# Kernel tuning notes

Measured on AMD Instinct MI355X. Metric: run time of the kernel, lower is better.

## Reference

```python
import jax, jax.numpy as jnp
import numpy as np
from jax.scipy.special import gammaln

N_L, N_Q, D_IN, D_CTX, H, MAX_AGENT = 256, 65536, 384, 192, 64, 6
STD2 = 0.1
VAR2 = STD2 * STD2
LOG_VAR2 = float(np.log(VAR2))
TEMP = 1.0


def _linear_init(k, out_dim, in_dim):
    k1, k2 = jax.random.split(k)
    s = 1.0 / np.sqrt(in_dim)
    w = jax.random.uniform(k1, (out_dim, in_dim), minval=-s, maxval=s, dtype=jnp.float32)
    b = jax.random.uniform(k2, (out_dim,), minval=-s, maxval=s, dtype=jnp.float32)
    return w, b


def setup_inputs() -> dict:
    key = jax.random.key(0)
    ks = jax.random.split(key, 12)
    fc1_w, fc1_b = _linear_init(ks[0], H, D_IN)
    fc21_w, fc21_b = _linear_init(ks[1], H, H)
    fc22_w, fc22_b = _linear_init(ks[2], H, H)
    fc3_w, fc3_b = _linear_init(ks[3], H, H)
    fc4_w, fc4_b = _linear_init(ks[4], D_IN, H)
    ctx_w, ctx_b = _linear_init(ks[5], H, D_CTX)
    llms = jax.random.normal(ks[6], (N_L, D_IN), dtype=jnp.float32)
    contexts = jax.random.normal(ks[7], (N_Q, D_CTX), dtype=jnp.float32)
    agent_num_int = jax.random.randint(ks[8], (N_Q, 1), 1, MAX_AGENT + 1, dtype=jnp.int32)
    agent_num_float = agent_num_int.astype(jnp.float32)
    noise_eps = jax.random.normal(ks[9], (N_L, H), dtype=jnp.float32)   # VAE reparameterize eps
    rand_u = jax.random.uniform(ks[10], (MAX_AGENT, N_Q, 1), dtype=jnp.float32)  # per-step uniforms
    return dict(llms=llms, contexts=contexts, agent_num_int=agent_num_int,
                agent_num_float=agent_num_float,
                fc1_w=fc1_w, fc1_b=fc1_b, fc21_w=fc21_w, fc21_b=fc21_b,
                fc22_w=fc22_w, fc22_b=fc22_b, fc3_w=fc3_w, fc3_b=fc3_b,
                fc4_w=fc4_w, fc4_b=fc4_b, ctx_w=ctx_w, ctx_b=ctx_b,
                noise_eps=noise_eps, rand_u=rand_u)


def _l2norm(x):
    n = jnp.sqrt(jnp.sum(x * x, axis=1, keepdims=True))
    return x / jnp.maximum(n, 1e-12)


def reference(llms, contexts, agent_num_int, agent_num_float,
              fc1_w, fc1_b, fc21_w, fc21_b, fc22_w, fc22_b,
              fc3_w, fc3_b, fc4_w, fc4_b, ctx_w, ctx_b, noise_eps, rand_u):
    # ---- VAE encode / reparameterize / decode ----
    h = jax.nn.relu(llms @ fc1_w.T + fc1_b)
    mu = h @ fc21_w.T + fc21_b
    log_var = h @ fc22_w.T + fc22_b
    std = jnp.exp(0.5 * log_var) * STD2
    z = mu + noise_eps * std
    h2 = jax.nn.relu(z @ fc3_w.T + fc3_b)
    x_hat = h2 @ fc4_w.T + fc4_b
    mse = jnp.mean((x_hat - llms) ** 2)
    kld = -0.5 * jnp.mean(1.0 - LOG_VAR2 + log_var - (mu ** 2 + jnp.exp(log_var)) / VAR2)
    vae_loss = mse + kld

    # ---- embeddings and routing scores ----
    llm_emb = _l2norm(z)                                   # [N_l, H]
    ctx_emb = _l2norm(contexts @ ctx_w.T + ctx_b)          # [N_q, H]
    scores = jax.nn.softmax((ctx_emb @ llm_emb.T) / TEMP, axis=1)  # [N_q, N_l]
    scores_cumsum = jnp.cumsum(scores, axis=1)

    # ---- vectorized max_agent-step categorical sampling ----
    # sel[i, q] = first llm where cumsum > u (inverse-CDF sampling), for step i
    sel = jnp.argmax(scores_cumsum[None, :, :] > rand_u, axis=2)          # [A, N_q]
    steps = jnp.arange(1, rand_u.shape[0] + 1, dtype=agent_num_int.dtype)
    mask = (agent_num_int[None, :, 0] >= steps[:, None]).astype(scores.dtype)  # [A, N_q]
    rows = jnp.broadcast_to(jnp.arange(scores.shape[0])[None, :], sel.shape)
    selected_llm = jnp.zeros_like(scores).at[rows, sel].add(mask)          # [N_q, N_l]

    log_probs = (gammaln(agent_num_float + 1.0)
                 - jnp.sum(gammaln(selected_llm + 1.0), axis=1, keepdims=True)
                 + jnp.sum(selected_llm * jnp.log(scores), axis=1, keepdims=True))
    return selected_llm, log_probs, vae_loss
```

## Files before the change

kernel.cpp:

```cpp
#include <hip/hip_runtime.h>

#define N_L 256
#define N_Q 65536
#define D_IN 384
#define D_CTX 192
#define HDIM 64
#define MAXA 6

typedef float v2f __attribute__((ext_vector_type(2)));

__device__ __forceinline__ v2f mk2(float a, float b) { v2f r; r.x = a; r.y = b; return r; }

__device__ __forceinline__ void fma4(float& acc, const float4& w, const float4& v) {
    acc = fmaf(w.x, v.x, acc);
    acc = fmaf(w.y, v.y, acc);
    acc = fmaf(w.z, v.z, acc);
    acc = fmaf(w.w, v.w, acc);
}

__device__ __forceinline__ float lgfact(int n) {
    return (n <= 1) ? 0.0f :
           (n == 2) ? 0.6931471805599453f :
           (n == 3) ? 1.7917594692280550f :
           (n == 4) ? 3.1780538303479458f :
           (n == 5) ? 4.7874917427820460f :
                      6.5792512120101010f;
}

template<int CTRL, int RM, bool BC>
__device__ __forceinline__ float dppz(float x) {
    return __int_as_float(__builtin_amdgcn_update_dpp(0, __float_as_int(x), CTRL, RM, 0xF, BC));
}
template<int CTRL, int RM>
__device__ __forceinline__ float dpps(float x) {
    int xi = __float_as_int(x);
    return __int_as_float(__builtin_amdgcn_update_dpp(xi, xi, CTRL, RM, 0xF, false));
}
__device__ __forceinline__ float wave_iscan(float t) {
    t += dppz<0x111, 0xF, true>(t);
    t += dppz<0x112, 0xF, true>(t);
    t += dppz<0x114, 0xF, true>(t);
    t += dppz<0x118, 0xF, true>(t);
    t += dppz<0x142, 0xA, false>(t);
    t += dppz<0x143, 0xC, false>(t);
    return t;
}
__device__ __forceinline__ float wave_max_l63(float m) {
    m = fmaxf(m, dpps<0x111, 0xF>(m));
    m = fmaxf(m, dpps<0x112, 0xF>(m));
    m = fmaxf(m, dpps<0x114, 0xF>(m));
    m = fmaxf(m, dpps<0x118, 0xF>(m));
    m = fmaxf(m, dpps<0x142, 0xA>(m));
    m = fmaxf(m, dpps<0x143, 0xC>(m));
    return m;
}
__device__ __forceinline__ float bc63(float x) {
    return __int_as_float(__builtin_amdgcn_readlane(__float_as_int(x), 63));
}

__device__ __forceinline__ void pk_fma_lo(v2f& d, v2f a, v2f b) {
    asm("v_pk_fma_f32 %0, %1, %2, %0 op_sel:[0,0,0] op_sel_hi:[1,0,1]"
        : "+v"(d) : "v"(a), "v"(b));
}
__device__ __forceinline__ void pk_fma_hi(v2f& d, v2f a, v2f b) {
    asm("v_pk_fma_f32 %0, %1, %2, %0 op_sel:[0,1,0] op_sel_hi:[1,1,1]"
        : "+v"(d) : "v"(a), "v"(b));
}

__global__ __launch_bounds__(64) void vae_kernel(
    const float* __restrict__ llms, const float* __restrict__ ctx_w,
    const float* __restrict__ fc1_w, const float* __restrict__ fc1_b,
    const float* __restrict__ fc21_w, const float* __restrict__ fc21_b,
    const float* __restrict__ fc22_w, const float* __restrict__ fc22_b,
    const float* __restrict__ fc3_w, const float* __restrict__ fc3_b,
    const float* __restrict__ fc4_w, const float* __restrict__ fc4_b,
    const float* __restrict__ eps,
    float* __restrict__ ctx_wP, float* __restrict__ embT,
    float* __restrict__ mse_row, float* __restrict__ kld_row)
{
    __shared__ __align__(16) float xs[D_IN];
    __shared__ __align__(16) float hs[HDIM];
    __shared__ __align__(16) float zs[HDIM];
    __shared__ __align__(16) float h2s[HDIM];
    const int r = blockIdx.x;
    const int j = threadIdx.x;

    {
        int f = r * 64 + j;
        if (f < D_CTX * HDIM) {
            int p = f >> 2, rr = f & 3;
            int jc = p & 63, k4 = p >> 6;
            ctx_wP[f] = ctx_w[jc * D_CTX + k4 * 4 + rr];
        }
    }

    for (int k = j; k < D_IN; k += 64) xs[k] = llms[r * D_IN + k];
    __syncthreads();

    float acc = fc1_b[j];
    {
        const float4* wr = (const float4*)(fc1_w + (size_t)j * D_IN);
        const float4* xr = (const float4*)xs;
        #pragma unroll 8
        for (int k4 = 0; k4 < D_IN / 4; ++k4) { fma4(acc, wr[k4], xr[k4]); }
    }
    float h = fmaxf(acc, 0.0f);
    hs[j] = h;
    __syncthreads();

    float mu = fc21_b[j], lv = fc22_b[j];
    {
        const float4* w1 = (const float4*)(fc21_w + (size_t)j * HDIM);
        const float4* w2 = (const float4*)(fc22_w + (size_t)j * HDIM);
        const float4* hr = (const float4*)hs;
        #pragma unroll
        for (int k4 = 0; k4 < HDIM / 4; ++k4) {
            float4 hh = hr[k4];
            fma4(mu, w1[k4], hh);
            fma4(lv, w2[k4], hh);
        }
    }
    float stdv = expf(0.5f * lv) * 0.1f;
    float z = fmaf(eps[r * HDIM + j], stdv, mu);

    float elv = expf(lv);
    float kt = (1.0f - (-4.60517018598809136f)) + lv - (mu * mu + elv) / 0.01f;
    float ks = kt;
    #pragma unroll
    for (int o = 32; o; o >>= 1) ks += __shfl_xor(ks, o);

    float zsq = z * z;
    #pragma unroll
    for (int o = 32; o; o >>= 1) zsq += __shfl_xor(zsq, o);
    float nrm = fmaxf(sqrtf(zsq), 1e-12f);
    embT[j * N_L + r] = z / nrm;
    zs[j] = z;
    __syncthreads();

    float a3 = fc3_b[j];
    {
        const float4* w3 = (const float4*)(fc3_w + (size_t)j * HDIM);
        const float4* zr = (const float4*)zs;
        #pragma unroll
        for (int k4 = 0; k4 < HDIM / 4; ++k4) { fma4(a3, w3[k4], zr[k4]); }
    }
    float h2 = fmaxf(a3, 0.0f);
    h2s[j] = h2;
    __syncthreads();

    float ms = 0.0f;
    const float4* h2r = (const float4*)h2s;
    #pragma unroll
    for (int m = 0; m < 6; ++m) {
        int o = j + 64 * m;
        float a4 = fc4_b[o];
        const float4* w4 = (const float4*)(fc4_w + (size_t)o * HDIM);
        #pragma unroll
        for (int k4 = 0; k4 < HDIM / 4; ++k4) { fma4(a4, w4[k4], h2r[k4]); }
        float d = a4 - xs[o];
        ms = fmaf(d, d, ms);
    }
    #pragma unroll
    for (int o = 32; o; o >>= 1) ms += __shfl_xor(ms, o);
    if (j == 0) { mse_row[r] = ms; kld_row[r] = ks; }
}

__global__ __launch_bounds__(256) void route_kernel(
    const float* __restrict__ contexts, const float* __restrict__ ctx_wP, const float* __restrict__ ctx_b,
    const float* __restrict__ embT, const int* __restrict__ agent_num, const float* __restrict__ rand_u,
    const float* __restrict__ mse_row, const float* __restrict__ kld_row,
    float* __restrict__ out_sel, float* __restrict__ out_lp, float* __restrict__ out_loss)
{
    __shared__ __align__(16) float lds[4][1536];

    const int tid = threadIdx.x;
    const int lane = tid & 63;
    const int widx = tid >> 6;
    const int l0 = lane << 2;

    const int g = blockIdx.x * 4 + widx;
    const int q0 = __builtin_amdgcn_readfirstlane(g << 3);
    float* myl = lds[widx];

    {
        float4* xls = (float4*)myl;
        const float4* cbase = (const float4*)contexts + (size_t)q0 * (D_CTX / 4);
        #pragma unroll
        for (int it = 0; it < 6; ++it) {
            int f = lane + it * 64;
            xls[f] = cbase[f];
        }
    }

    if (g == 0) {
        int rr = lane * 4;
        float ms = mse_row[rr] + mse_row[rr + 1] + mse_row[rr + 2] + mse_row[rr + 3];
        float ks = kld_row[rr] + kld_row[rr + 1] + kld_row[rr + 2] + kld_row[rr + 3];
        #pragma unroll
        for (int o = 32; o; o >>= 1) { ms += __shfl_xor(ms, o); ks += __shfl_xor(ks, o); }
        if (lane == 0) out_loss[0] = ms / 98304.0f - 0.5f * (ks / 16384.0f);
    }

    int Aq[8];
    #pragma unroll
    for (int q = 0; q < 8; ++q) Aq[q] = agent_num[q0 + q];

    const float bj = ctx_b[lane];
    v2f acc[8];
    #pragma unroll
    for (int q = 0; q < 8; ++q) acc[q] = mk2(bj, 0.0f);
    {
        const float4* wp = (const float4*)ctx_wP;
        const float4* xls = (const float4*)myl;
        #pragma unroll 2
        for (int k4 = 0; k4 < D_CTX / 4; ++k4) {
            float4 w = wp[k4 * HDIM + lane];
            v2f w01 = mk2(w.x, w.y), w23 = mk2(w.z, w.w);
            #pragma unroll
            for (int q = 0; q < 8; ++q) {
                float4 xv = xls[q * 48 + k4];
                acc[q] = __builtin_elementwise_fma(w01, mk2(xv.x, xv.y), acc[q]);
                acc[q] = __builtin_elementwise_fma(w23, mk2(xv.z, xv.w), acc[q]);
            }
        }
    }
    float e[8];
    #pragma unroll
    for (int q = 0; q < 8; ++q) e[q] = acc[q].x + acc[q].y;
    #pragma unroll
    for (int q = 0; q < 8; ++q) {
        float s = bc63(wave_iscan(e[q] * e[q]));
        e[q] *= 1.0f / fmaxf(sqrtf(s), 1e-12f);
        myl[q * HDIM + lane] = e[q];
    }

    v2f Pa[8], Pb[8];
    #pragma unroll
    for (int q = 0; q < 8; ++q) { Pa[q] = mk2(0.0f, 0.0f); Pb[q] = mk2(0.0f, 0.0f); }

    #pragma unroll 2
    for (int j4 = 0; j4 < HDIM / 4; ++j4) {
        float4 M0 = *(const float4*)(embT + (size_t)(j4 * 4 + 0) * N_L + l0);
        float4 M1 = *(const float4*)(embT + (size_t)(j4 * 4 + 1) * N_L + l0);
        float4 M2 = *(const float4*)(embT + (size_t)(j4 * 4 + 2) * N_L + l0);
        float4 M3 = *(const float4*)(embT + (size_t)(j4 * 4 + 3) * N_L + l0);
        v2f m0a = mk2(M0.x, M0.y), m0b = mk2(M0.z, M0.w);
        v2f m1a = mk2(M1.x, M1.y), m1b = mk2(M1.z, M1.w);
        v2f m2a = mk2(M2.x, M2.y), m2b = mk2(M2.z, M2.w);
        v2f m3a = mk2(M3.x, M3.y), m3b = mk2(M3.z, M3.w);
        #pragma unroll
        for (int q = 0; q < 8; ++q) {
            float4 ev = *(const float4*)(myl + q * HDIM + j4 * 4);
            v2f e01 = mk2(ev.x, ev.y), e23 = mk2(ev.z, ev.w);
            pk_fma_lo(Pa[q], m0a, e01);
            pk_fma_hi(Pa[q], m1a, e01);
            pk_fma_lo(Pa[q], m2a, e23);
            pk_fma_hi(Pa[q], m3a, e23);
            pk_fma_lo(Pb[q], m0b, e01);
            pk_fma_hi(Pb[q], m1b, e01);
            pk_fma_lo(Pb[q], m2b, e23);
            pk_fma_hi(Pb[q], m3b, e23);
        }
    }

    float4 P[8];
    #pragma unroll
    for (int k = 0; k < 8; ++k) P[k] = make_float4(Pa[k].x, Pa[k].y, Pb[k].x, Pb[k].y);

    #pragma unroll
    for (int k = 0; k < 8; ++k) {
        float m = fmaxf(fmaxf(P[k].x, P[k].y), fmaxf(P[k].z, P[k].w));
        m = bc63(wave_max_l63(m));
        P[k].x = expf(P[k].x - m); P[k].y = expf(P[k].y - m);
        P[k].z = expf(P[k].z - m); P[k].w = expf(P[k].w - m);
        float s = bc63(wave_iscan(P[k].x + P[k].y + P[k].z + P[k].w));
        float inv = 1.0f / s;
        P[k].x *= inv; P[k].y *= inv; P[k].z *= inv; P[k].w *= inv;
    }

    float c0[8], c1[8], c2[8], c3[8];
    #pragma unroll
    for (int k = 0; k < 8; ++k) {
        c0[k] = P[k].x; c1[k] = c0[k] + P[k].y; c2[k] = c1[k] + P[k].z;
        float p3 = c2[k] + P[k].w;
        float t = wave_iscan(p3);
        float base = t - p3;
        c0[k] += base; c1[k] += base; c2[k] += base; c3[k] = p3 + base;
    }

    unsigned nib[8] = {0, 0, 0, 0, 0, 0, 0, 0};
    #pragma unroll
    for (int i = 0; i < MAXA; ++i) {
        #pragma unroll
        for (int k = 0; k < 8; ++k) {
            if (i < Aq[k]) {
                float u = rand_u[(size_t)i * N_Q + q0 + k];
                unsigned long long b0 = __ballot(c0[k] <= u);
                unsigned long long b1 = __ballot(c1[k] <= u);
                unsigned long long b2 = __ballot(c2[k] <= u);
                unsigned long long b3 = __ballot(c3[k] <= u);
                int loc = __popcll(b0) + __popcll(b1) + __popcll(b2) + __popcll(b3);
                int sel = (loc >= N_L) ? 0 : loc;
                unsigned d = (unsigned)(sel - l0);
                if (d < 4u) nib[k] += 1u << (4 * d);
            }
        }
    }

    float term[8];
    #pragma unroll
    for (int k = 0; k < 8; ++k) {
        int n0 = nib[k] & 15, n1 = (nib[k] >> 4) & 15, n2 = (nib[k] >> 8) & 15, n3 = (nib[k] >> 12) & 15;
        float4 rowv = make_float4((float)n0, (float)n1, (float)n2, (float)n3);
        *(((float4*)(out_sel + (size_t)(q0 + k) * N_L)) + lane) = rowv;
        float tm = 0.0f;
        if (n0) tm += (float)n0 * logf(P[k].x) - lgfact(n0);
        if (n1) tm += (float)n1 * logf(P[k].y) - lgfact(n1);
        if (n2) tm += (float)n2 * logf(P[k].z) - lgfact(n2);
        if (n3) tm += (float)n3 * logf(P[k].w) - lgfact(n3);
        term[k] = tm;
    }
    float st[8];
    #pragma unroll
    for (int k = 0; k < 8; ++k) st[k] = bc63(wave_iscan(term[k]));

    if (lane < 8) {
        float rr = st[0];
        int Aa = Aq[0];
        #pragma unroll
        for (int k = 1; k < 8; ++k) {
            if (lane == k) { rr = st[k]; Aa = Aq[k]; }
        }
        out_lp[q0 + lane] = lgfact(Aa) + rr;
    }
}

extern "C" void kernel_launch(void* const* d_in, const int* in_sizes, int n_in,
                              void* d_out, int out_size, void* d_ws, size_t ws_size,
                              hipStream_t stream) {
    const float* llms      = (const float*)d_in[0];
    const float* contexts  = (const float*)d_in[1];
    const int*   agent_i   = (const int*)  d_in[2];
    const float* fc1_w  = (const float*)d_in[4];  const float* fc1_b  = (const float*)d_in[5];
    const float* fc21_w = (const float*)d_in[6];  const float* fc21_b = (const float*)d_in[7];
    const float* fc22_w = (const float*)d_in[8];  const float* fc22_b = (const float*)d_in[9];
    const float* fc3_w  = (const float*)d_in[10]; const float* fc3_b  = (const float*)d_in[11];
    const float* fc4_w  = (const float*)d_in[12]; const float* fc4_b  = (const float*)d_in[13];
    const float* ctx_w  = (const float*)d_in[14]; const float* ctx_b  = (const float*)d_in[15];
    const float* noise  = (const float*)d_in[16]; const float* rand_u = (const float*)d_in[17];

    float* out      = (float*)d_out;
    float* out_sel  = out;
    float* out_lp   = out + (size_t)N_Q * N_L;
    float* out_loss = out_lp + N_Q;

    float* ctx_wP   = (float*)d_ws;
    float* embT     = ctx_wP + D_CTX * HDIM;
    float* mse_row  = embT + HDIM * N_L;
    float* kld_row  = mse_row + N_L;

    vae_kernel<<<N_L, 64, 0, stream>>>(llms, ctx_w, fc1_w, fc1_b, fc21_w, fc21_b, fc22_w, fc22_b,
                                       fc3_w, fc3_b, fc4_w, fc4_b, noise,
                                       ctx_wP, embT, mse_row, kld_row);
    route_kernel<<<2048, 256, 0, stream>>>(contexts, ctx_wP, ctx_b, embT, agent_i, rand_u,
                                           mse_row, kld_row, out_sel, out_lp, out_loss);
}
```

Before: 228.7 us.

## Halve route kernel LDS staging and recompute probabilities from cumsum to raise occupancy

```diff
diff --git a/kernel.cpp b/kernel.cpp
--- a/kernel.cpp
+++ b/kernel.cpp
@@ -165,13 +165,13 @@
     if (j == 0) { mse_row[r] = ms; kld_row[r] = ks; }
 }
 
-__global__ __launch_bounds__(256) void route_kernel(
+__global__ __launch_bounds__(256, 8) void route_kernel(
     const float* __restrict__ contexts, const float* __restrict__ ctx_wP, const float* __restrict__ ctx_b,
     const float* __restrict__ embT, const int* __restrict__ agent_num, const float* __restrict__ rand_u,
     const float* __restrict__ mse_row, const float* __restrict__ kld_row,
     float* __restrict__ out_sel, float* __restrict__ out_lp, float* __restrict__ out_loss)
 {
-    __shared__ __align__(16) float lds[4][1536];
+    __shared__ __align__(16) float lds[4][768];
 
     const int tid = threadIdx.x;
     const int lane = tid & 63;
@@ -182,15 +182,13 @@
     const int q0 = __builtin_amdgcn_readfirstlane(g << 3);
     float* myl = lds[widx];
 
-    {
-        float4* xls = (float4*)myl;
-        const float4* cbase = (const float4*)contexts + (size_t)q0 * (D_CTX / 4);
-        #pragma unroll
-        for (int it = 0; it < 6; ++it) {
-            int f = lane + it * 64;
-            xls[f] = cbase[f];
-        }
-    }
+    float4* xls = (float4*)myl;
+    const float4* cbase = (const float4*)contexts + (size_t)q0 * (D_CTX / 4);
+    #pragma unroll
+    for (int it = 0; it < 3; ++it) xls[lane + it * 64] = cbase[lane + it * 64];
+    float4 xh1[3];
+    #pragma unroll
+    for (int it = 0; it < 3; ++it) xh1[it] = cbase[192 + lane + it * 64];
 
     if (g == 0) {
         int rr = lane * 4;
@@ -211,16 +209,28 @@
     for (int q = 0; q < 8; ++q) acc[q] = mk2(bj, 0.0f);
     {
         const float4* wp = (const float4*)ctx_wP;
-        const float4* xls = (const float4*)myl;
         #pragma unroll 2
         for (int k4 = 0; k4 < D_CTX / 4; ++k4) {
             float4 w = wp[k4 * HDIM + lane];
             v2f w01 = mk2(w.x, w.y), w23 = mk2(w.z, w.w);
             #pragma unroll
-            for (int q = 0; q < 8; ++q) {
+            for (int q = 0; q < 4; ++q) {
                 float4 xv = xls[q * 48 + k4];
                 acc[q] = __builtin_elementwise_fma(w01, mk2(xv.x, xv.y), acc[q]);
                 acc[q] = __builtin_elementwise_fma(w23, mk2(xv.z, xv.w), acc[q]);
+            }
+        }
+        #pragma unroll
+        for (int it = 0; it < 3; ++it) xls[lane + it * 64] = xh1[it];
+        #pragma unroll 2
+        for (int k4 = 0; k4 < D_CTX / 4; ++k4) {
+            float4 w = wp[k4 * HDIM + lane];
+            v2f w01 = mk2(w.x, w.y), w23 = mk2(w.z, w.w);
+            #pragma unroll
+            for (int q = 0; q < 4; ++q) {
+                float4 xv = xls[q * 48 + k4];
+                acc[4 + q] = __builtin_elementwise_fma(w01, mk2(xv.x, xv.y), acc[4 + q]);
+                acc[4 + q] = __builtin_elementwise_fma(w23, mk2(xv.z, xv.w), acc[4 + q]);
             }
         }
     }
@@ -263,26 +273,19 @@
         }
     }
 
-    float4 P[8];
-    #pragma unroll
-    for (int k = 0; k < 8; ++k) P[k] = make_float4(Pa[k].x, Pa[k].y, Pb[k].x, Pb[k].y);
-
+    float c0[8], c1[8], c2[8], c3[8];
     #pragma unroll
     for (int k = 0; k < 8; ++k) {
-        float m = fmaxf(fmaxf(P[k].x, P[k].y), fmaxf(P[k].z, P[k].w));
+        float px = Pa[k].x, py = Pa[k].y, pz = Pb[k].x, pw = Pb[k].y;
+        float m = fmaxf(fmaxf(px, py), fmaxf(pz, pw));
         m = bc63(wave_max_l63(m));
-        P[k].x = expf(P[k].x - m); P[k].y = expf(P[k].y - m);
-        P[k].z = expf(P[k].z - m); P[k].w = expf(P[k].w - m);
-        float s = bc63(wave_iscan(P[k].x + P[k].y + P[k].z + P[k].w));
+        px = expf(px - m); py = expf(py - m);
+        pz = expf(pz - m); pw = expf(pw - m);
+        float s = bc63(wave_iscan(px + py + pz + pw));
         float inv = 1.0f / s;
-        P[k].x *= inv; P[k].y *= inv; P[k].z *= inv; P[k].w *= inv;
-    }
-
-    float c0[8], c1[8], c2[8], c3[8];
-    #pragma unroll
-    for (int k = 0; k < 8; ++k) {
-        c0[k] = P[k].x; c1[k] = c0[k] + P[k].y; c2[k] = c1[k] + P[k].z;
-        float p3 = c2[k] + P[k].w;
+        px *= inv; py *= inv; pz *= inv; pw *= inv;
+        c0[k] = px; c1[k] = c0[k] + py; c2[k] = c1[k] + pz;
+        float p3 = c2[k] + pw;
         float t = wave_iscan(p3);
         float base = t - p3;
         c0[k] += base; c1[k] += base; c2[k] += base; c3[k] = p3 + base;
@@ -313,11 +316,14 @@
         int n0 = nib[k] & 15, n1 = (nib[k] >> 4) & 15, n2 = (nib[k] >> 8) & 15, n3 = (nib[k] >> 12) & 15;
         float4 rowv = make_float4((float)n0, (float)n1, (float)n2, (float)n3);
         *(((float4*)(out_sel + (size_t)(q0 + k) * N_L)) + lane) = rowv;
+        float base = __shfl_up(c3[k], 1);
+        base = (lane == 0) ? 0.0f : base;
+        float px = c0[k] - base, py = c1[k] - c0[k], pz = c2[k] - c1[k], pw = c3[k] - c2[k];
         float tm = 0.0f;
-        if (n0) tm += (float)n0 * logf(P[k].x) - lgfact(n0);
-        if (n1) tm += (float)n1 * logf(P[k].y) - lgfact(n1);
-        if (n2) tm += (float)n2 * logf(P[k].z) - lgfact(n2);
-        if (n3) tm += (float)n3 * logf(P[k].w) - lgfact(n3);
+        if (n0) tm += (float)n0 * logf(px) - lgfact(n0);
+        if (n1) tm += (float)n1 * logf(py) - lgfact(n1);
+        if (n2) tm += (float)n2 * logf(pz) - lgfact(n2);
+        if (n3) tm += (float)n3 * logf(pw) - lgfact(n3);
         term[k] = tm;
     }
     float st[8];
```

Result: no change. 231.0 us (+1.0%).
